# Kernel optimization log

Hardware: AMD Instinct MI355X
Metric: run time of the kernel (lower is better)

The kernel has to match this reference:

```python
import jax, jax.numpy as jnp
import numpy as np
import math

WS = 8       # window_size
NH = 4       # num_heads
D = 256      # d_model
B = 16
HH = 64
WW = 64
EPS = 1e-5


def _sincos_pe(ws, d):
    pe = np.zeros((ws * ws, d), np.float32)
    dh = d // 2
    y = np.repeat(np.arange(ws), ws).astype(np.float32)
    x = np.tile(np.arange(ws), ws).astype(np.float32)
    div = np.exp(np.arange(0, dh, 2).astype(np.float32) * (-math.log(10000.0) / dh))
    pe[:, 0:dh:2] = np.sin(y[:, None] * div)
    pe[:, 1:dh:2] = np.cos(y[:, None] * div)
    pe[:, dh::2] = np.sin(x[:, None] * div)
    pe[:, dh + 1::2] = np.cos(x[:, None] * div)
    return jnp.asarray(pe)[None]  # [1, ws*ws, d]


def setup_inputs() -> dict:
    key = jax.random.key(0)
    ks = iter(jax.random.split(key, 32))
    rnd = lambda *s: jax.random.normal(next(ks), s, dtype=jnp.float32) * 0.02
    inp = {
        'feat_A': jax.random.normal(next(ks), (B, HH * WW, D), dtype=jnp.float32),
        'feat_B': jax.random.normal(next(ks), (B, HH * WW, D), dtype=jnp.float32),
        'local_pe': _sincos_pe(WS, D),
    }
    for s in ('A', 'B'):
        inp[f'qkv_w_{s}'] = rnd(3, D, D)
        inp[f'qkv_b_{s}'] = rnd(3, D)
        inp[f'out_w_{s}'] = rnd(D, D)
        inp[f'out_b_{s}'] = rnd(D)
        inp[f'norm_g_{s}'] = jnp.ones((D,), jnp.float32)
        inp[f'norm_b_{s}'] = jnp.zeros((D,), jnp.float32)
        inp[f'ffn_norm_g_{s}'] = jnp.ones((D,), jnp.float32)
        inp[f'ffn_norm_b_{s}'] = jnp.zeros((D,), jnp.float32)
        inp[f'ffn_w1_{s}'] = rnd(2 * D, D)
        inp[f'ffn_b1_{s}'] = rnd(2 * D)
        inp[f'ffn_w2_{s}'] = rnd(D, 2 * D)
        inp[f'ffn_b2_{s}'] = rnd(D)
    inp['H'] = HH
    inp['W'] = WW
    return inp


def _partition(x, H, W):
    # [B, H*W, C] -> [B*nW, WS*WS, C]; H, W assumed divisible by WS (no pad branch)
    b, _, c = x.shape
    x = x.reshape(b, H // WS, WS, W // WS, WS, c)
    return x.transpose(0, 1, 3, 2, 4, 5).reshape(-1, WS * WS, c)


def _reverse(w, b, H, W):
    c = w.shape[-1]
    x = w.reshape(b, H // WS, W // WS, WS, WS, c)
    return x.transpose(0, 1, 3, 2, 4, 5).reshape(b, H * W, c)


def _ln(x, g, b):
    m = jnp.mean(x, -1, keepdims=True)
    v = jnp.mean(jnp.square(x - m), -1, keepdims=True)
    return (x - m) * jax.lax.rsqrt(v + EPS) * g + b


def _mha(q_in, kv_in, qkv_w, qkv_b, out_w, out_b):
    s, c = q_in.shape[1], q_in.shape[2]
    dh = c // NH
    q = (q_in @ qkv_w[0].T + qkv_b[0]).reshape(-1, s, NH, dh)
    k = (kv_in @ qkv_w[1].T + qkv_b[1]).reshape(-1, s, NH, dh)
    v = (kv_in @ qkv_w[2].T + qkv_b[2]).reshape(-1, s, NH, dh)
    attn = jax.nn.softmax(jnp.einsum('bqhd,bkhd->bhqk', q, k) / math.sqrt(dh), axis=-1)
    o = jnp.einsum('bhqk,bkhd->bqhd', attn, v).reshape(-1, s, c)
    return o @ out_w.T + out_b


def _ffn(x, w1, b1, w2, b2):
    return jax.nn.gelu(x @ w1.T + b1, approximate=False) @ w2.T + b2


def reference(feat_A, feat_B, local_pe,
              qkv_w_A, qkv_b_A, out_w_A, out_b_A,
              qkv_w_B, qkv_b_B, out_w_B, out_b_B,
              norm_g_A, norm_b_A, ffn_norm_g_A, ffn_norm_b_A,
              ffn_w1_A, ffn_b1_A, ffn_w2_A, ffn_b2_A,
              norm_g_B, norm_b_B, ffn_norm_g_B, ffn_norm_b_B,
              ffn_w1_B, ffn_b1_B, ffn_w2_B, ffn_b2_B,
              H, W):
    b = feat_A.shape[0]
    sc_A, sc_B = feat_A, feat_B
    win_A = _partition(feat_A, H, W) + local_pe
    win_B = _partition(feat_B, H, W) + local_pe
    attn_A = _mha(win_A, win_B, qkv_w_A, qkv_b_A, out_w_A, out_b_A)
    attn_B = _mha(win_B, win_A, qkv_w_B, qkv_b_B, out_w_B, out_b_B)
    fA = _reverse(attn_A, b, H, W)
    fB = _reverse(attn_B, b, H, W)
    fA = _ln(fA + sc_A, norm_g_A, norm_b_A)
    fA = _ln(fA + _ffn(fA, ffn_w1_A, ffn_b1_A, ffn_w2_A, ffn_b2_A), ffn_norm_g_A, ffn_norm_b_A)
    fB = _ln(fB + sc_B, norm_g_B, norm_b_B)
    fB = _ln(fB + _ffn(fB, ffn_w1_B, ffn_b1_B, ffn_w2_B, ffn_b2_B), ffn_norm_g_B, ffn_norm_b_B)
    return (fA, fB)
```

## Files before the change

### kernel.cpp

```cpp
#include <hip/hip_runtime.h>
#include <hip/hip_bf16.h>
#include <math.h>

typedef __bf16 bf16;
typedef __bf16 bf16x8 __attribute__((ext_vector_type(8)));
typedef __bf16 bf16x4 __attribute__((ext_vector_type(4)));
typedef float f32x4 __attribute__((ext_vector_type(4)));

#define NTOK 65536
#define DMODEL 256

#define GL16(g, l) __builtin_amdgcn_global_load_lds( \
    (const __attribute__((address_space(1))) void*)(g), \
    (__attribute__((address_space(3))) void*)(l), 16, 0, 0)

__device__ __forceinline__ int unwin_idx(int m) {
    int widx = m >> 6, t = m & 63;
    int b = widx >> 6, wl = widx & 63;
    return (b << 12) | (((wl >> 3) * 8 + (t >> 3)) << 6) | ((wl & 7) * 8 + (t & 7));
}

__device__ __forceinline__ float gelu_fast(float x) {
    float z = 0.7978845608f * (x + 0.044715f * x * x * x);
    float e = __expf(2.f * z);
    float t = (e - 1.f) / (e + 1.f);
    return 0.5f * x * (1.f + t);
}

__global__ __launch_bounds__(256)
void prep_win(const float* __restrict__ fA, const float* __restrict__ fB,
              const float* __restrict__ pe,
              bf16* __restrict__ awA, bf16* __restrict__ awB)
{
    const float* f = blockIdx.y ? fB : fA;
    bf16* aw = blockIdx.y ? awB : awA;
    int m = blockIdx.x * 8 + (threadIdx.x >> 5);
    int c = (threadIdx.x & 31) * 8;
    int g = unwin_idx(m), t = m & 63;
    const float4* fs = reinterpret_cast<const float4*>(f + (size_t)g * 256 + c);
    const float4* ps = reinterpret_cast<const float4*>(pe + t * 256 + c);
    float4 a0 = fs[0], a1 = fs[1], p0 = ps[0], p1 = ps[1];
    bf16x8 o;
    o[0] = (bf16)(a0.x + p0.x); o[1] = (bf16)(a0.y + p0.y);
    o[2] = (bf16)(a0.z + p0.z); o[3] = (bf16)(a0.w + p0.w);
    o[4] = (bf16)(a1.x + p1.x); o[5] = (bf16)(a1.y + p1.y);
    o[6] = (bf16)(a1.z + p1.z); o[7] = (bf16)(a1.w + p1.w);
    *reinterpret_cast<bf16x8*>(aw + (size_t)m * 256 + c) = o;
}

__global__ __launch_bounds__(256)
void cvt8(const float* __restrict__ s0, const float* __restrict__ s1,
          const float* __restrict__ s2, const float* __restrict__ s3,
          const float* __restrict__ s4, const float* __restrict__ s5,
          const float* __restrict__ s6, const float* __restrict__ s7,
          bf16* __restrict__ d)
{
    int idx = (blockIdx.x * 256 + threadIdx.x) * 4;
    const float* s; int off;
    if      (idx < 196608) { s = s0; off = 0; }
    else if (idx < 262144) { s = s1; off = 196608; }
    else if (idx < 393216) { s = s2; off = 262144; }
    else if (idx < 524288) { s = s3; off = 393216; }
    else if (idx < 720896) { s = s4; off = 524288; }
    else if (idx < 786432) { s = s5; off = 720896; }
    else if (idx < 917504) { s = s6; off = 786432; }
    else                   { s = s7; off = 917504; }
    float4 v = *reinterpret_cast<const float4*>(s + (idx - off));
    bf16x4 o; o[0] = (bf16)v.x; o[1] = (bf16)v.y; o[2] = (bf16)v.z; o[3] = (bf16)v.w;
    *reinterpret_cast<bf16x4*>(d + idx) = o;
}

__global__ __launch_bounds__(256, 4)
void gemm_qkv2(const bf16* __restrict__ awA, const bf16* __restrict__ awB,
               const bf16* __restrict__ wA, const bf16* __restrict__ wB,
               const float* __restrict__ bA, const float* __restrict__ bB,
               bf16* __restrict__ qA, bf16* __restrict__ kA, bf16* __restrict__ vA,
               bf16* __restrict__ qB, bf16* __restrict__ kB, bf16* __restrict__ vB)
{
    __shared__ bf16 As[2][4096];
    __shared__ bf16 Bs[2][4096];
    const int tid = threadIdx.x;
    const int bx = blockIdx.x;
    const int xcd = bx & 7, slot = bx >> 3;
    const int L = xcd * 768 + slot;
    const int mt = L / 6, nb = L - mt * 6;
    const int pass = mt >> 9, mb = mt & 511;
    const int seg = nb >> 1, nl0 = (nb & 1) * 128;
    const int m0 = mb * 128;

    const bf16* A = pass ? awB : awA;
    const bf16* Wf = (seg == 0) ? (pass ? wB : wA) : (pass ? wA : wB);
    const float* Bf = (seg == 0) ? (pass ? bB : bA) : (pass ? bA : bB);
    const bf16* W = Wf + (size_t)seg * 65536;
    const float* bia = Bf + seg * 256;
    bf16* qout = pass ? qB : qA;
    bf16* kout = pass ? kA : kB;
    bf16* vout = pass ? vA : vB;

    const int lane = tid & 63, w = tid >> 6;
    const int wr = w >> 1, wc = w & 1;
    const int lr = lane & 15, lg = lane >> 4;
    const int srow = tid >> 2, scol = (tid & 3) * 8;

    const bf16* Ag = A + (size_t)(m0 + srow) * 256 + scol;
    const bf16* Bg = W + (size_t)(nl0 + srow) * 256 + scol;

    f32x4 acc[4][4];
    const f32x4 zero = {0.f, 0.f, 0.f, 0.f};
#pragma unroll
    for (int mi = 0; mi < 4; ++mi)
#pragma unroll
        for (int nj = 0; nj < 4; ++nj) acc[mi][nj] = zero;

    auto stage = [&](int buf, int k0) {
        GL16(Ag + k0, &As[buf][tid * 8]);
        GL16(Ag + 64 * 256 + k0, &As[buf][2048 + tid * 8]);
        GL16(Bg + k0, &Bs[buf][tid * 8]);
        GL16(Bg + 64 * 256 + k0, &Bs[buf][2048 + tid * 8]);
    };
    auto compute = [&](int buf) {
        bf16x8 af[4], bfr[4];
#pragma unroll
        for (int mi = 0; mi < 4; ++mi)
            af[mi] = *reinterpret_cast<const bf16x8*>(&As[buf][(wr * 64 + mi * 16 + lr) * 32 + lg * 8]);
#pragma unroll
        for (int nj = 0; nj < 4; ++nj)
            bfr[nj] = *reinterpret_cast<const bf16x8*>(&Bs[buf][(wc * 64 + nj * 16 + lr) * 32 + lg * 8]);
#pragma unroll
        for (int mi = 0; mi < 4; ++mi)
#pragma unroll
            for (int nj = 0; nj < 4; ++nj)
                acc[mi][nj] = __builtin_amdgcn_mfma_f32_16x16x32_bf16(af[mi], bfr[nj], acc[mi][nj], 0, 0, 0);
    };

    stage(0, 0);
    __syncthreads();
#pragma unroll
    for (int t = 0; t < 7; ++t) {
        stage((t + 1) & 1, (t + 1) * 32);
        compute(t & 1);
        __syncthreads();
    }
    compute(1);

    if (seg == 2) {
        const int widx = mb * 2 + wr;
#pragma unroll
        for (int nj = 0; nj < 4; ++nj) {
            int cl = nl0 + wc * 64 + nj * 16 + lr;
            float bv = bia[cl];
#pragma unroll
            for (int mi = 0; mi < 4; ++mi) {
                bf16x4 o;
#pragma unroll
                for (int i = 0; i < 4; ++i) o[i] = (bf16)(acc[mi][nj][i] + bv);
                *reinterpret_cast<bf16x4*>(vout + ((size_t)widx * 256 + cl) * 64 + mi * 16 + lg * 4) = o;
            }
        }
    } else {
        bf16* out = (seg == 0) ? qout : kout;
#pragma unroll
        for (int nj = 0; nj < 4; ++nj) {
            int cl = nl0 + wc * 64 + nj * 16 + lr;
            float bv = bia[cl];
#pragma unroll
            for (int mi = 0; mi < 4; ++mi)
#pragma unroll
                for (int i = 0; i < 4; ++i) {
                    int row = m0 + wr * 64 + mi * 16 + lg * 4 + i;
                    out[(size_t)row * 256 + cl] = (bf16)(acc[mi][nj][i] + bv);
                }
        }
    }
}

__global__ __launch_bounds__(256, 4)
void gemm_gelu(const bf16* __restrict__ y1A, const bf16* __restrict__ y1B,
               const bf16* __restrict__ wA, const bf16* __restrict__ wB,
               const float* __restrict__ bA, const float* __restrict__ bB,
               bf16* __restrict__ hbA, bf16* __restrict__ hbB)
{
    __shared__ bf16 As[2][4096];
    __shared__ bf16 Bs[2][4096];
    const int tid = threadIdx.x;
    const int bx = blockIdx.x;
    const int xcd = bx & 7, slot = bx >> 3;
    const int L = xcd * 512 + slot;
    const int mt = L >> 2, nb = L & 3;
    const int str = mt >> 9, mb = mt & 511;
    const int m0 = mb * 128, n0 = nb * 128;

    const bf16* A = str ? y1B : y1A;
    const bf16* W = str ? wB : wA;
    const float* bia = str ? bB : bA;
    bf16* C = str ? hbB : hbA;

    const int lane = tid & 63, w = tid >> 6;
    const int wr = w >> 1, wc = w & 1;
    const int lr = lane & 15, lg = lane >> 4;
    const int srow = tid >> 2, scol = (tid & 3) * 8;

    const bf16* Ag = A + (size_t)(m0 + srow) * 256 + scol;
    const bf16* Bg = W + (size_t)(n0 + srow) * 256 + scol;

    f32x4 acc[4][4];
    const f32x4 zero = {0.f, 0.f, 0.f, 0.f};
#pragma unroll
    for (int mi = 0; mi < 4; ++mi)
#pragma unroll
        for (int nj = 0; nj < 4; ++nj) acc[mi][nj] = zero;

    auto stage = [&](int buf, int k0) {
        GL16(Ag + k0, &As[buf][tid * 8]);
        GL16(Ag + 64 * 256 + k0, &As[buf][2048 + tid * 8]);
        GL16(Bg + k0, &Bs[buf][tid * 8]);
        GL16(Bg + 64 * 256 + k0, &Bs[buf][2048 + tid * 8]);
    };
    auto compute = [&](int buf) {
        bf16x8 af[4], bfr[4];
#pragma unroll
        for (int mi = 0; mi < 4; ++mi)
            af[mi] = *reinterpret_cast<const bf16x8*>(&As[buf][(wr * 64 + mi * 16 + lr) * 32 + lg * 8]);
#pragma unroll
        for (int nj = 0; nj < 4; ++nj)
            bfr[nj] = *reinterpret_cast<const bf16x8*>(&Bs[buf][(wc * 64 + nj * 16 + lr) * 32 + lg * 8]);
#pragma unroll
        for (int mi = 0; mi < 4; ++mi)
#pragma unroll
            for (int nj = 0; nj < 4; ++nj)
                acc[mi][nj] = __builtin_amdgcn_mfma_f32_16x16x32_bf16(af[mi], bfr[nj], acc[mi][nj], 0, 0, 0);
    };

    stage(0, 0);
    __syncthreads();
#pragma unroll
    for (int t = 0; t < 7; ++t) {
        stage((t + 1) & 1, (t + 1) * 32);
        compute(t & 1);
        __syncthreads();
    }
    compute(1);

#pragma unroll
    for (int nj = 0; nj < 4; ++nj) {
        int col = n0 + wc * 64 + nj * 16 + lr;
        float bv = bia[col];
#pragma unroll
        for (int mi = 0; mi < 4; ++mi)
#pragma unroll
            for (int i = 0; i < 4; ++i) {
                int row = m0 + wr * 64 + mi * 16 + lg * 4 + i;
                C[(size_t)row * 512 + col] = (bf16)gelu_fast(acc[mi][nj][i] + bv);
            }
    }
}

template<int UNWIN>
__global__ __launch_bounds__(512, 4)
void gemm_lnr(const bf16* __restrict__ A0, const bf16* __restrict__ A1,
              const bf16* __restrict__ W0, const bf16* __restrict__ W1,
              const float* __restrict__ bias0, const float* __restrict__ bias1,
              const float* __restrict__ rf0, const float* __restrict__ rf1,
              const bf16* __restrict__ rb0, const bf16* __restrict__ rb1,
              const float* __restrict__ g0, const float* __restrict__ g1,
              const float* __restrict__ be0, const float* __restrict__ be1,
              float* __restrict__ of0, float* __restrict__ of1,
              bf16* __restrict__ ob0, bf16* __restrict__ ob1, int K)
{
    __shared__ bf16 As[2][4096];
    __shared__ bf16 Bs[2][8192];
    __shared__ float redS[4][128];
    __shared__ float redQ[4][128];
    const int tid = threadIdx.x;
    const int bx = blockIdx.x;
    const int str = bx >> 9, mb = bx & 511;
    const int m0 = mb * 128;

    const bf16* A = str ? A1 : A0;
    const bf16* W = str ? W1 : W0;
    const float* bias = str ? bias1 : bias0;
    const float* resf = str ? rf1 : rf0;
    const bf16* resb = str ? rb1 : rb0;
    const float* gamma = str ? g1 : g0;
    const float* beta = str ? be1 : be0;
    float* outf = str ? of1 : of0;
    bf16* outb = str ? ob1 : ob0;

    const int lane = tid & 63, w = tid >> 6;
    const int wr = w >> 2, wc = w & 3;
    const int lr = lane & 15, lg = lane >> 4;
    const int srow = tid >> 2, scol = (tid & 3) * 8;

    const bf16* Ag = A + (size_t)(m0 + srow) * K + scol;
    const bf16* Bg0 = W + (size_t)srow * K + scol;
    const bf16* Bg1 = W + (size_t)(128 + srow) * K + scol;

    f32x4 acc[4][4];
    const f32x4 zero = {0.f, 0.f, 0.f, 0.f};
#pragma unroll
    for (int mi = 0; mi < 4; ++mi)
#pragma unroll
        for (int nj = 0; nj < 4; ++nj) acc[mi][nj] = zero;

    auto stage = [&](int buf, int k0) {
        GL16(Ag + k0, &As[buf][tid * 8]);
        GL16(Bg0 + k0, &Bs[buf][tid * 8]);
        GL16(Bg1 + k0, &Bs[buf][4096 + tid * 8]);
    };
    auto compute = [&](int buf) {
        bf16x8 af[4], bfr[4];
#pragma unroll
        for (int mi = 0; mi < 4; ++mi)
            af[mi] = *reinterpret_cast<const bf16x8*>(&As[buf][(wr * 64 + mi * 16 + lr) * 32 + lg * 8]);
#pragma unroll
        for (int nj = 0; nj < 4; ++nj)
            bfr[nj] = *reinterpret_cast<const bf16x8*>(&Bs[buf][(wc * 64 + nj * 16 + lr) * 32 + lg * 8]);
#pragma unroll
        for (int mi = 0; mi < 4; ++mi)
#pragma unroll
            for (int nj = 0; nj < 4; ++nj)
                acc[mi][nj] = __builtin_amdgcn_mfma_f32_16x16x32_bf16(af[mi], bfr[nj], acc[mi][nj], 0, 0, 0);
    };

    const int NT = K >> 5;
    stage(0, 0);
    __syncthreads();
    for (int t = 0; t < NT - 1; ++t) {
        stage((t + 1) & 1, (t + 1) * 32);
        compute(t & 1);
        __syncthreads();
    }
    compute((NT - 1) & 1);

    float bsv[4], gv[4], bvv[4];
    int cols[4];
#pragma unroll
    for (int nj = 0; nj < 4; ++nj) {
        cols[nj] = wc * 64 + nj * 16 + lr;
        bsv[nj] = bias[cols[nj]];
        gv[nj] = gamma[cols[nj]];
        bvv[nj] = beta[cols[nj]];
    }
    int grow[4][4];
#pragma unroll
    for (int mi = 0; mi < 4; ++mi)
#pragma unroll
        for (int i = 0; i < 4; ++i) {
            int m = m0 + wr * 64 + mi * 16 + lg * 4 + i;
            grow[mi][i] = UNWIN ? unwin_idx(m) : m;
        }

#pragma unroll
    for (int mi = 0; mi < 4; ++mi)
#pragma unroll
        for (int i = 0; i < 4; ++i) {
            float ls = 0.f, lq = 0.f;
#pragma unroll
            for (int nj = 0; nj < 4; ++nj) {
                float rv;
                if (UNWIN) rv = resf[(size_t)grow[mi][i] * 256 + cols[nj]];
                else       rv = (float)resb[(size_t)grow[mi][i] * 256 + cols[nj]];
                float v = acc[mi][nj][i] + bsv[nj] + rv;
                acc[mi][nj][i] = v;
                ls += v;
                lq += v * v;
            }
            ls += __shfl_xor(ls, 1); lq += __shfl_xor(lq, 1);
            ls += __shfl_xor(ls, 2); lq += __shfl_xor(lq, 2);
            ls += __shfl_xor(ls, 4); lq += __shfl_xor(lq, 4);
            ls += __shfl_xor(ls, 8); lq += __shfl_xor(lq, 8);
            if (lr == 0) {
                int rloc = wr * 64 + mi * 16 + lg * 4 + i;
                redS[wc][rloc] = ls;
                redQ[wc][rloc] = lq;
            }
        }
    __syncthreads();

#pragma unroll
    for (int mi = 0; mi < 4; ++mi)
#pragma unroll
        for (int i = 0; i < 4; ++i) {
            int rloc = wr * 64 + mi * 16 + lg * 4 + i;
            float S = redS[0][rloc] + redS[1][rloc] + redS[2][rloc] + redS[3][rloc];
            float Q = redQ[0][rloc] + redQ[1][rloc] + redQ[2][rloc] + redQ[3][rloc];
            float mean = S * (1.f / 256.f);
            float var = Q * (1.f / 256.f) - mean * mean;
            float rstd = rsqrtf(var + 1e-5f);
#pragma unroll
            for (int nj = 0; nj < 4; ++nj) {
                float o = (acc[mi][nj][i] - mean) * rstd * gv[nj] + bvv[nj];
                if (UNWIN) outb[(size_t)grow[mi][i] * 256 + cols[nj]] = (bf16)o;
                else       outf[(size_t)grow[mi][i] * 256 + cols[nj]] = o;
            }
        }
}

__global__ __launch_bounds__(256)
void attn_win2(const bf16* qA, const bf16* __restrict__ kA,
               const bf16* __restrict__ vA,
               const bf16* qB, const bf16* __restrict__ kB,
               const bf16* __restrict__ vB)
{
    __shared__ bf16 Ps[4][64][72];
    const int tid = threadIdx.x;
    const int wv = tid >> 6, lane = tid & 63;
    const int str = blockIdx.x >> 10, widx = blockIdx.x & 1023, head = wv;
    const int lr = lane & 15, lg = lane >> 4;
    const bf16* qbuf = str ? qB : qA;
    const bf16* kbuf = str ? kB : kA;
    const bf16* vtbuf = str ? vB : vA;
    bf16* obuf = const_cast<bf16*>(qbuf);
    const bf16* qb = qbuf + (size_t)widx * 64 * 256 + head * 64;
    const bf16* kb = kbuf + (size_t)widx * 64 * 256 + head * 64;
    const bf16* vb = vtbuf + (size_t)widx * 16384 + head * 64 * 64;

    const f32x4 zero = {0.f, 0.f, 0.f, 0.f};
    f32x4 sacc[4][4];
#pragma unroll
    for (int mi = 0; mi < 4; ++mi)
#pragma unroll
        for (int nj = 0; nj < 4; ++nj) sacc[mi][nj] = zero;

#pragma unroll
    for (int k0 = 0; k0 < 64; k0 += 32) {
        bf16x8 af[4], bfr[4];
#pragma unroll
        for (int mi = 0; mi < 4; ++mi)
            af[mi] = *reinterpret_cast<const bf16x8*>(qb + (size_t)(mi * 16 + lr) * 256 + k0 + lg * 8);
#pragma unroll
        for (int nj = 0; nj < 4; ++nj)
            bfr[nj] = *reinterpret_cast<const bf16x8*>(kb + (size_t)(nj * 16 + lr) * 256 + k0 + lg * 8);
#pragma unroll
        for (int mi = 0; mi < 4; ++mi)
#pragma unroll
            for (int nj = 0; nj < 4; ++nj)
                sacc[mi][nj] = __builtin_amdgcn_mfma_f32_16x16x32_bf16(af[mi], bfr[nj], sacc[mi][nj], 0, 0, 0);
    }

    const float c = 0.125f * 1.4426950408889634f;
    float rsum[4][4];
#pragma unroll
    for (int mi = 0; mi < 4; ++mi)
#pragma unroll
        for (int i = 0; i < 4; ++i) {
            float m = fmaxf(fmaxf(sacc[mi][0][i], sacc[mi][1][i]), fmaxf(sacc[mi][2][i], sacc[mi][3][i]));
            m = fmaxf(m, __shfl_xor(m, 1));
            m = fmaxf(m, __shfl_xor(m, 2));
            m = fmaxf(m, __shfl_xor(m, 4));
            m = fmaxf(m, __shfl_xor(m, 8));
#pragma unroll
            for (int nj = 0; nj < 4; ++nj)
                sacc[mi][nj][i] = exp2f((sacc[mi][nj][i] - m) * c);
            float s = sacc[mi][0][i] + sacc[mi][1][i] + sacc[mi][2][i] + sacc[mi][3][i];
            s += __shfl_xor(s, 1);
            s += __shfl_xor(s, 2);
            s += __shfl_xor(s, 4);
            s += __shfl_xor(s, 8);
            rsum[mi][i] = s;
        }

#pragma unroll
    for (int mi = 0; mi < 4; ++mi)
#pragma unroll
        for (int nj = 0; nj < 4; ++nj)
#pragma unroll
            for (int i = 0; i < 4; ++i)
                Ps[wv][mi * 16 + lg * 4 + i][nj * 16 + lr] = (bf16)sacc[mi][nj][i];

    f32x4 oacc[4][4];
#pragma unroll
    for (int mi = 0; mi < 4; ++mi)
#pragma unroll
        for (int nj = 0; nj < 4; ++nj) oacc[mi][nj] = zero;
#pragma unroll
    for (int k0 = 0; k0 < 64; k0 += 32) {
        bf16x8 af[4], bfr[4];
#pragma unroll
        for (int mi = 0; mi < 4; ++mi)
            af[mi] = *reinterpret_cast<const bf16x8*>(&Ps[wv][mi * 16 + lr][k0 + lg * 8]);
#pragma unroll
        for (int nj = 0; nj < 4; ++nj)
            bfr[nj] = *reinterpret_cast<const bf16x8*>(vb + (size_t)(nj * 16 + lr) * 64 + k0 + lg * 8);
#pragma unroll
        for (int mi = 0; mi < 4; ++mi)
#pragma unroll
            for (int nj = 0; nj < 4; ++nj)
                oacc[mi][nj] = __builtin_amdgcn_mfma_f32_16x16x32_bf16(af[mi], bfr[nj], oacc[mi][nj], 0, 0, 0);
    }
#pragma unroll
    for (int mi = 0; mi < 4; ++mi)
#pragma unroll
        for (int i = 0; i < 4; ++i) {
            float inv = 1.0f / rsum[mi][i];
            int row = mi * 16 + lg * 4 + i;
#pragma unroll
            for (int nj = 0; nj < 4; ++nj)
                obuf[((size_t)widx * 64 + row) * 256 + head * 64 + nj * 16 + lr] =
                    (bf16)(oacc[mi][nj][i] * inv);
        }
}

extern "C" void kernel_launch(void* const* d_in, const int* in_sizes, int n_in,
                              void* d_out, int out_size, void* d_ws, size_t ws_size,
                              hipStream_t stream)
{
    const float* feat_A       = (const float*)d_in[0];
    const float* feat_B       = (const float*)d_in[1];
    const float* pe           = (const float*)d_in[2];
    const float* qkv_w_A      = (const float*)d_in[3];
    const float* qkv_b_A      = (const float*)d_in[4];
    const float* out_w_A      = (const float*)d_in[5];
    const float* out_b_A      = (const float*)d_in[6];
    const float* norm_g_A     = (const float*)d_in[7];
    const float* norm_b_A     = (const float*)d_in[8];
    const float* ffn_norm_g_A = (const float*)d_in[9];
    const float* ffn_norm_b_A = (const float*)d_in[10];
    const float* ffn_w1_A     = (const float*)d_in[11];
    const float* ffn_b1_A     = (const float*)d_in[12];
    const float* ffn_w2_A     = (const float*)d_in[13];
    const float* ffn_b2_A     = (const float*)d_in[14];
    const float* qkv_w_B      = (const float*)d_in[15];
    const float* qkv_b_B      = (const float*)d_in[16];
    const float* out_w_B      = (const float*)d_in[17];
    const float* out_b_B      = (const float*)d_in[18];
    const float* norm_g_B     = (const float*)d_in[19];
    const float* norm_b_B     = (const float*)d_in[20];
    const float* ffn_norm_g_B = (const float*)d_in[21];
    const float* ffn_norm_b_B = (const float*)d_in[22];
    const float* ffn_w1_B     = (const float*)d_in[23];
    const float* ffn_b1_B     = (const float*)d_in[24];
    const float* ffn_w2_B     = (const float*)d_in[25];
    const float* ffn_b2_B     = (const float*)d_in[26];

    char* ws = (char*)d_ws;
    const size_t BFE = (size_t)NTOK * DMODEL;
    const size_t BFB = BFE * 2;

    bf16* Wb = (bf16*)ws;
    size_t off = 2u * 1024 * 1024;
    bf16* awA = (bf16*)(ws + off); off += BFB;
    bf16* awB = (bf16*)(ws + off); off += BFB;
    bf16* qA  = (bf16*)(ws + off); off += BFB;
    bf16* kA  = (bf16*)(ws + off); off += BFB;
    bf16* vA  = (bf16*)(ws + off); off += BFB;
    bf16* qB  = (bf16*)(ws + off); off += BFB;
    bf16* kB  = (bf16*)(ws + off); off += BFB;
    bf16* vB  = (bf16*)(ws + off); off += BFB;
    bf16* hbA = awA;
    bf16* hbB = kA;
    bf16* y1A = kB;
    bf16* y1B = vB;

    bf16* w_qkvA = Wb + 0;
    bf16* w_outA = Wb + 196608;
    bf16* w_f1A  = Wb + 262144;
    bf16* w_f2A  = Wb + 393216;
    bf16* w_qkvB = Wb + 524288;
    bf16* w_outB = Wb + 720896;
    bf16* w_f1B  = Wb + 786432;
    bf16* w_f2B  = Wb + 917504;

    cvt8<<<1024, 256, 0, stream>>>(qkv_w_A, out_w_A, ffn_w1_A, ffn_w2_A,
                                   qkv_w_B, out_w_B, ffn_w1_B, ffn_w2_B, Wb);
    prep_win<<<dim3(8192, 2), 256, 0, stream>>>(feat_A, feat_B, pe, awA, awB);

    gemm_qkv2<<<6144, 256, 0, stream>>>(awA, awB, w_qkvA, w_qkvB,
                                        qkv_b_A, qkv_b_B,
                                        qA, kA, vA, qB, kB, vB);

    attn_win2<<<2048, 256, 0, stream>>>(qA, kA, vA, qB, kB, vB);

    gemm_lnr<1><<<1024, 512, 0, stream>>>(qA, qB, w_outA, w_outB,
                                          out_b_A, out_b_B,
                                          feat_A, feat_B, nullptr, nullptr,
                                          norm_g_A, norm_g_B, norm_b_A, norm_b_B,
                                          nullptr, nullptr, y1A, y1B, 256);
    gemm_gelu<<<4096, 256, 0, stream>>>(y1A, y1B, w_f1A, w_f1B,
                                        ffn_b1_A, ffn_b1_B, hbA, hbB);
    gemm_lnr<0><<<1024, 512, 0, stream>>>(hbA, hbB, w_f2A, w_f2B,
                                          ffn_b2_A, ffn_b2_B,
                                          nullptr, nullptr, y1A, y1B,
                                          ffn_norm_g_A, ffn_norm_g_B,
                                          ffn_norm_b_A, ffn_norm_b_B,
                                          (float*)d_out, (float*)d_out + BFE,
                                          nullptr, nullptr, 512);
}
```

Measured before the change: 498.6 us.

## Split fused GEMM+LayerNorm into tiled GEMM and standalone LayerNorm kernels

Replaces the 512-thread GEMM that computed full 256-wide rows and fused bias, residual and LayerNorm with two kernels. The first is a 128x128-tile GEMM (256 threads, XCD-aware block mapping) that writes bias-added bf16 results. The second is a row-wise LayerNorm kernel that adds the residual and normalizes. The aim is smaller tiles and higher occupancy in the GEMM. The cost is an extra bf16 round trip through global memory and two more kernel launches.

```diff
diff --git a/kernel.cpp b/kernel.cpp
--- a/kernel.cpp
+++ b/kernel.cpp
@@ -255,145 +255,153 @@
     }
 }
 
-template<int UNWIN>
-__global__ __launch_bounds__(512, 4)
-void gemm_lnr(const bf16* __restrict__ A0, const bf16* __restrict__ A1,
+template<int WK, int UNWIN>
+__global__ __launch_bounds__(256, 4)
+void gemm_out(const bf16* __restrict__ A0, const bf16* __restrict__ A1,
               const bf16* __restrict__ W0, const bf16* __restrict__ W1,
-              const float* __restrict__ bias0, const float* __restrict__ bias1,
-              const float* __restrict__ rf0, const float* __restrict__ rf1,
-              const bf16* __restrict__ rb0, const bf16* __restrict__ rb1,
-              const float* __restrict__ g0, const float* __restrict__ g1,
-              const float* __restrict__ be0, const float* __restrict__ be1,
-              float* __restrict__ of0, float* __restrict__ of1,
-              bf16* __restrict__ ob0, bf16* __restrict__ ob1, int K)
+              const float* __restrict__ b0, const float* __restrict__ b1,
+              bf16* __restrict__ C0, bf16* __restrict__ C1)
 {
     __shared__ bf16 As[2][4096];
-    __shared__ bf16 Bs[2][8192];
-    __shared__ float redS[4][128];
-    __shared__ float redQ[4][128];
+    __shared__ bf16 Bs[2][4096];
     const int tid = threadIdx.x;
     const int bx = blockIdx.x;
-    const int str = bx >> 9, mb = bx & 511;
-    const int m0 = mb * 128;
+    const int xcd = bx & 7, slot = bx >> 3;
+    const int L = xcd * 256 + slot;
+    const int mt = L >> 1, nb = L & 1;
+    const int str = mt >> 9, mb = mt & 511;
+    const int m0 = mb * 128, n0 = nb * 128;
 
     const bf16* A = str ? A1 : A0;
     const bf16* W = str ? W1 : W0;
-    const float* bias = str ? bias1 : bias0;
-    const float* resf = str ? rf1 : rf0;
-    const bf16* resb = str ? rb1 : rb0;
+    const float* bia = str ? b1 : b0;
+    bf16* C = str ? C1 : C0;
+
+    const int lane = tid & 63, w = tid >> 6;
+    const int wr = w >> 1, wc = w & 1;
+    const int lr = lane & 15, lg = lane >> 4;
+    const int srow = tid >> 2, scol = (tid & 3) * 8;
+
+    const bf16* Ag = A + (size_t)(m0 + srow) * WK + scol;
+    const bf16* Bg = W + (size_t)(n0 + srow) * WK + scol;
+
+    f32x4 acc[4][4];
+    const f32x4 zero = {0.f, 0.f, 0.f, 0.f};
+#pragma unroll
+    for (int mi = 0; mi < 4; ++mi)
+#pragma unroll
+        for (int nj = 0; nj < 4; ++nj) acc[mi][nj] = zero;
+
+    auto stage = [&](int buf, int k0) {
+        GL16(Ag + k0, &As[buf][tid * 8]);
+        GL16(Ag + (size_t)64 * WK + k0, &As[buf][2048 + tid * 8]);
+        GL16(Bg + k0, &Bs[buf][tid * 8]);
+        GL16(Bg + (size_t)64 * WK + k0, &Bs[buf][2048 + tid * 8]);
+    };
+    auto compute = [&](int buf) {
+        bf16x8 af[4], bfr[4];
+#pragma unroll
+        for (int mi = 0; mi < 4; ++mi)
+            af[mi] = *reinterpret_cast<const bf16x8*>(&As[buf][(wr * 64 + mi * 16 + lr) * 32 + lg * 8]);
+#pragma unroll
+        for (int nj = 0; nj < 4; ++nj)
+            bfr[nj] = *reinterpret_cast<const bf16x8*>(&Bs[buf][(wc * 64 + nj * 16 + lr) * 32 + lg * 8]);
+#pragma unroll
+        for (int mi = 0; mi < 4; ++mi)
+#pragma unroll
+            for (int nj = 0; nj < 4; ++nj)
+                acc[mi][nj] = __builtin_amdgcn_mfma_f32_16x16x32_bf16(af[mi], bfr[nj], acc[mi][nj], 0, 0, 0);
+    };
+
+    const int NT = WK / 32;
+    stage(0, 0);
+    __syncthreads();
+#pragma unroll
+    for (int t = 0; t < NT - 1; ++t) {
+        stage((t + 1) & 1, (t + 1) * 32);
+        compute(t & 1);
+        __syncthreads();
+    }
+    compute((NT - 1) & 1);
+
+#pragma unroll
+    for (int nj = 0; nj < 4; ++nj) {
+        int col = n0 + wc * 64 + nj * 16 + lr;
+        float bv = bia[col];
+#pragma unroll
+        for (int mi = 0; mi < 4; ++mi)
+#pragma unroll
+            for (int i = 0; i < 4; ++i) {
+                int row = m0 + wr * 64 + mi * 16 + lg * 4 + i;
+                int gr = UNWIN ? unwin_idx(row) : row;
+                C[(size_t)gr * 256 + col] = (bf16)(acc[mi][nj][i] + bv);
+            }
+    }
+}
+
+template<int RESF, int OUTF>
+__global__ __launch_bounds__(256)
+void ln_fz(const bf16* __restrict__ x0, const bf16* __restrict__ x1,
+           const float* __restrict__ rf0, const float* __restrict__ rf1,
+           const bf16* __restrict__ rb0, const bf16* __restrict__ rb1,
+           const float* __restrict__ g0, const float* __restrict__ g1,
+           const float* __restrict__ be0, const float* __restrict__ be1,
+           float* __restrict__ of0, float* __restrict__ of1,
+           bf16* __restrict__ ob0, bf16* __restrict__ ob1)
+{
+    const int bx = blockIdx.x;
+    const int str = bx >> 14, b = bx & 16383;
+    const bf16* x = str ? x1 : x0;
+    const float* rf = str ? rf1 : rf0;
+    const bf16* rb = str ? rb1 : rb0;
     const float* gamma = str ? g1 : g0;
     const float* beta = str ? be1 : be0;
     float* outf = str ? of1 : of0;
     bf16* outb = str ? ob1 : ob0;
 
-    const int lane = tid & 63, w = tid >> 6;
-    const int wr = w >> 2, wc = w & 3;
-    const int lr = lane & 15, lg = lane >> 4;
-    const int srow = tid >> 2, scol = (tid & 3) * 8;
-
-    const bf16* Ag = A + (size_t)(m0 + srow) * K + scol;
-    const bf16* Bg0 = W + (size_t)srow * K + scol;
-    const bf16* Bg1 = W + (size_t)(128 + srow) * K + scol;
-
-    f32x4 acc[4][4];
-    const f32x4 zero = {0.f, 0.f, 0.f, 0.f};
-#pragma unroll
-    for (int mi = 0; mi < 4; ++mi)
-#pragma unroll
-        for (int nj = 0; nj < 4; ++nj) acc[mi][nj] = zero;
-
-    auto stage = [&](int buf, int k0) {
-        GL16(Ag + k0, &As[buf][tid * 8]);
-        GL16(Bg0 + k0, &Bs[buf][tid * 8]);
-        GL16(Bg1 + k0, &Bs[buf][4096 + tid * 8]);
-    };
-    auto compute = [&](int buf) {
-        bf16x8 af[4], bfr[4];
-#pragma unroll
-        for (int mi = 0; mi < 4; ++mi)
-            af[mi] = *reinterpret_cast<const bf16x8*>(&As[buf][(wr * 64 + mi * 16 + lr) * 32 + lg * 8]);
-#pragma unroll
-        for (int nj = 0; nj < 4; ++nj)
-            bfr[nj] = *reinterpret_cast<const bf16x8*>(&Bs[buf][(wc * 64 + nj * 16 + lr) * 32 + lg * 8]);
-#pragma unroll
-        for (int mi = 0; mi < 4; ++mi)
-#pragma unroll
-            for (int nj = 0; nj < 4; ++nj)
-                acc[mi][nj] = __builtin_amdgcn_mfma_f32_16x16x32_bf16(af[mi], bfr[nj], acc[mi][nj], 0, 0, 0);
-    };
-
-    const int NT = K >> 5;
-    stage(0, 0);
-    __syncthreads();
-    for (int t = 0; t < NT - 1; ++t) {
-        stage((t + 1) & 1, (t + 1) * 32);
-        compute(t & 1);
-        __syncthreads();
-    }
-    compute((NT - 1) & 1);
-
-    float bsv[4], gv[4], bvv[4];
-    int cols[4];
-#pragma unroll
-    for (int nj = 0; nj < 4; ++nj) {
-        cols[nj] = wc * 64 + nj * 16 + lr;
-        bsv[nj] = bias[cols[nj]];
-        gv[nj] = gamma[cols[nj]];
-        bvv[nj] = beta[cols[nj]];
-    }
-    int grow[4][4];
-#pragma unroll
-    for (int mi = 0; mi < 4; ++mi)
-#pragma unroll
-        for (int i = 0; i < 4; ++i) {
-            int m = m0 + wr * 64 + mi * 16 + lg * 4 + i;
-            grow[mi][i] = UNWIN ? unwin_idx(m) : m;
-        }
-
-#pragma unroll
-    for (int mi = 0; mi < 4; ++mi)
-#pragma unroll
-        for (int i = 0; i < 4; ++i) {
-            float ls = 0.f, lq = 0.f;
-#pragma unroll
-            for (int nj = 0; nj < 4; ++nj) {
-                float rv;
-                if (UNWIN) rv = resf[(size_t)grow[mi][i] * 256 + cols[nj]];
-                else       rv = (float)resb[(size_t)grow[mi][i] * 256 + cols[nj]];
-                float v = acc[mi][nj][i] + bsv[nj] + rv;
-                acc[mi][nj][i] = v;
-                ls += v;
-                lq += v * v;
-            }
-            ls += __shfl_xor(ls, 1); lq += __shfl_xor(lq, 1);
-            ls += __shfl_xor(ls, 2); lq += __shfl_xor(lq, 2);
-            ls += __shfl_xor(ls, 4); lq += __shfl_xor(lq, 4);
-            ls += __shfl_xor(ls, 8); lq += __shfl_xor(lq, 8);
-            if (lr == 0) {
-                int rloc = wr * 64 + mi * 16 + lg * 4 + i;
-                redS[wc][rloc] = ls;
-                redQ[wc][rloc] = lq;
-            }
-        }
-    __syncthreads();
-
-#pragma unroll
-    for (int mi = 0; mi < 4; ++mi)
-#pragma unroll
-        for (int i = 0; i < 4; ++i) {
-            int rloc = wr * 64 + mi * 16 + lg * 4 + i;
-            float S = redS[0][rloc] + redS[1][rloc] + redS[2][rloc] + redS[3][rloc];
-            float Q = redQ[0][rloc] + redQ[1][rloc] + redQ[2][rloc] + redQ[3][rloc];
-            float mean = S * (1.f / 256.f);
-            float var = Q * (1.f / 256.f) - mean * mean;
-            float rstd = rsqrtf(var + 1e-5f);
-#pragma unroll
-            for (int nj = 0; nj < 4; ++nj) {
-                float o = (acc[mi][nj][i] - mean) * rstd * gv[nj] + bvv[nj];
-                if (UNWIN) outb[(size_t)grow[mi][i] * 256 + cols[nj]] = (bf16)o;
-                else       outf[(size_t)grow[mi][i] * 256 + cols[nj]] = o;
-            }
-        }
+    int row = b * 4 + (threadIdx.x >> 6);
+    int lane = threadIdx.x & 63;
+    size_t base = (size_t)row * 256 + lane * 4;
+    bf16x4 xv = *reinterpret_cast<const bf16x4*>(x + base);
+    float v[4];
+    if (RESF) {
+        float4 rv = *reinterpret_cast<const float4*>(rf + base);
+        v[0] = rv.x + (float)xv[0];
+        v[1] = rv.y + (float)xv[1];
+        v[2] = rv.z + (float)xv[2];
+        v[3] = rv.w + (float)xv[3];
+    } else {
+        bf16x4 rv = *reinterpret_cast<const bf16x4*>(rb + base);
+        v[0] = (float)rv[0] + (float)xv[0];
+        v[1] = (float)rv[1] + (float)xv[1];
+        v[2] = (float)rv[2] + (float)xv[2];
+        v[3] = (float)rv[3] + (float)xv[3];
+    }
+    float s = v[0] + v[1] + v[2] + v[3];
+    float q = v[0] * v[0] + v[1] * v[1] + v[2] * v[2] + v[3] * v[3];
+#pragma unroll
+    for (int m = 1; m < 64; m <<= 1) {
+        s += __shfl_xor(s, m);
+        q += __shfl_xor(q, m);
+    }
+    float mean = s * (1.f / 256.f);
+    float var = q * (1.f / 256.f) - mean * mean;
+    float rstd = rsqrtf(var + 1e-5f);
+    float4 gv = *reinterpret_cast<const float4*>(gamma + lane * 4);
+    float4 bv = *reinterpret_cast<const float4*>(beta + lane * 4);
+    float o[4];
+    o[0] = (v[0] - mean) * rstd * gv.x + bv.x;
+    o[1] = (v[1] - mean) * rstd * gv.y + bv.y;
+    o[2] = (v[2] - mean) * rstd * gv.z + bv.z;
+    o[3] = (v[3] - mean) * rstd * gv.w + bv.w;
+    if (OUTF) {
+        float4 ov; ov.x = o[0]; ov.y = o[1]; ov.z = o[2]; ov.w = o[3];
+        *reinterpret_cast<float4*>(outf + base) = ov;
+    } else {
+        bf16x4 ob;
+        ob[0] = (bf16)o[0]; ob[1] = (bf16)o[1]; ob[2] = (bf16)o[2]; ob[3] = (bf16)o[3];
+        *reinterpret_cast<bf16x4*>(outb + base) = ob;
+    }
 }
 
 __global__ __launch_bounds__(256)
@@ -534,7 +542,7 @@
     const float* ffn_b2_B     = (const float*)d_in[26];
 
     char* ws = (char*)d_ws;
-    const size_t BFE = (size_t)NTOK * DMODEL;
+    const size_t BFE = (size_t)NTOK * 256;
     const size_t BFB = BFE * 2;
 
     bf16* Wb = (bf16*)ws;
@@ -547,10 +555,14 @@
     bf16* qB  = (bf16*)(ws + off); off += BFB;
     bf16* kB  = (bf16*)(ws + off); off += BFB;
     bf16* vB  = (bf16*)(ws + off); off += BFB;
+    bf16* tb1A = kA;
+    bf16* tb1B = vA;
+    bf16* y1A = kB;
+    bf16* y1B = vB;
     bf16* hbA = awA;
     bf16* hbB = kA;
-    bf16* y1A = kB;
-    bf16* y1B = vB;
+    bf16* tb2A = qA;
+    bf16* tb2B = qB;
 
     bf16* w_qkvA = Wb + 0;
     bf16* w_outA = Wb + 196608;
@@ -571,18 +583,20 @@
 
     attn_win2<<<2048, 256, 0, stream>>>(qA, kA, vA, qB, kB, vB);
 
-    gemm_lnr<1><<<1024, 512, 0, stream>>>(qA, qB, w_outA, w_outB,
-                                          out_b_A, out_b_B,
-                                          feat_A, feat_B, nullptr, nullptr,
-                                          norm_g_A, norm_g_B, norm_b_A, norm_b_B,
-                                          nullptr, nullptr, y1A, y1B, 256);
+    gemm_out<256, 1><<<2048, 256, 0, stream>>>(qA, qB, w_outA, w_outB,
+                                               out_b_A, out_b_B, tb1A, tb1B);
+    ln_fz<1, 0><<<32768, 256, 0, stream>>>(tb1A, tb1B, feat_A, feat_B,
+                                           nullptr, nullptr,
+                                           norm_g_A, norm_g_B, norm_b_A, norm_b_B,
+                                           nullptr, nullptr, y1A, y1B);
     gemm_gelu<<<4096, 256, 0, stream>>>(y1A, y1B, w_f1A, w_f1B,
                                         ffn_b1_A, ffn_b1_B, hbA, hbB);
-    gemm_lnr<0><<<1024, 512, 0, stream>>>(hbA, hbB, w_f2A, w_f2B,
-                                          ffn_b2_A, ffn_b2_B,
-                                          nullptr, nullptr, y1A, y1B,
-                                          ffn_norm_g_A, ffn_norm_g_B,
-                                          ffn_norm_b_A, ffn_norm_b_B,
-                                          (float*)d_out, (float*)d_out + BFE,
-                                          nullptr, nullptr, 512);
-}
+    gemm_out<512, 0><<<2048, 256, 0, stream>>>(hbA, hbB, w_f2A, w_f2B,
+                                               ffn_b2_A, ffn_b2_B, tb2A, tb2B);
+    ln_fz<0, 1><<<32768, 256, 0, stream>>>(tb2A, tb2B, nullptr, nullptr,
+                                           y1A, y1B,
+                                           ffn_norm_g_A, ffn_norm_g_B,
+                                           ffn_norm_b_A, ffn_norm_b_B,
+                                           (float*)d_out, (float*)d_out + BFE,
+                                           nullptr, nullptr);
+}
```

After: 511.1 us. 1.03x slower.
